# Optimization experiments

Measured on AMD Instinct MI355X. Metric: run time of the kernel, lower is better.

## Reference

```python
import jax, jax.numpy as jnp
import numpy as np

SCALE, Z, X, Y = 4, 9, 9, 9
INV_SQRT_2PI = 1.0 / np.sqrt(2.0 * np.pi)


def setup_inputs() -> dict:
    key = jax.random.key(0)
    k1, = jax.random.split(key, 1)
    inp = jax.random.normal(k1, (1, 1, 128, 512, 512), dtype=jnp.float32)
    return {
        "inp": inp,
        "mu_z": jnp.asarray(0.0, dtype=jnp.float32),
        "sig_z": jnp.asarray(0.1, dtype=jnp.float32),
        "bet_xy": jnp.asarray(2.0, dtype=jnp.float32),
        "bet_z": jnp.asarray(1.5, dtype=jnp.float32),
    }


def _gen_alf(bet_xy, bet_z):
    # squared distances along each axis; torch's loop overwrites the wrap-around
    # write, so the net result for odd sizes is simply (arange - size//2)**2
    zd = ((jnp.arange(Z) - Z // 2) ** 2).astype(jnp.float32)[:, None, None]
    xd = ((jnp.arange(X) - X // 2) ** 2).astype(jnp.float32)[None, :, None]
    yd = ((jnp.arange(Y) - Y // 2) ** 2).astype(jnp.float32)[None, None, :]
    d_2 = zd / bet_z ** 2 + (xd + yd) / bet_xy ** 2  # (Z, X, Y)
    return jnp.exp(-d_2 / 2) * INV_SQRT_2PI


def reference(inp, mu_z, sig_z, bet_xy, bet_z):
    z0 = jnp.exp(mu_z + 0.5 * sig_z ** 2)
    rec = inp * z0  # (N, 1, D, H, W)
    alf = _gen_alf(bet_xy, bet_z)[None, None]  # (1, 1, Z, X, Y)
    pad_z = (Z - SCALE + 1) // 2
    rec = jax.lax.conv_general_dilated(
        rec, alf,
        window_strides=(SCALE, 1, 1),
        padding=[(pad_z, pad_z), (X // 2, X // 2), (Y // 2, Y // 2)],
        dimension_numbers=("NCDHW", "OIDHW", "NCDHW"),
    )  # (N, 1, D//SCALE, H, W)
    rec = (rec - rec.min()) / (rec.max() - rec.min())
    return rec
```

## Files before the change

kernel.cpp:

```cpp
#include <hip/hip_runtime.h>

#define D_IN  128
#define D_OUT 32
#define H     512
#define W     512
#define W4    128
#define HB    8
#define ZR    (HB + 8)
#define NTHR  512
#define CONV_GRID (D_OUT * (H / HB))

__global__ __launch_bounds__(NTHR)
void conv3d_fused(const float* __restrict__ inp, float* __restrict__ out,
                  const float* __restrict__ bxy_p, const float* __restrict__ bz_p,
                  float* __restrict__ blkMin, float* __restrict__ blkMax) {
    __shared__ float zbuf[ZR * W];
    __shared__ float smin[8], smax[8];

    const int d  = blockIdx.x >> 6;
    const int h0 = (blockIdx.x & 63) * HB;

    const float bz = bz_p[0], bx = bxy_p[0];
    const float iz = 1.0f / (2.0f * bz * bz);
    const float ix = 1.0f / (2.0f * bx * bx);
    float wz[9], wx[9];
#pragma unroll
    for (int k = 0; k < 9; ++k) {
        float dd = (float)(k - 4);
        wz[k] = expf(-dd * dd * iz);
        wx[k] = expf(-dd * dd * ix);
    }

    const float4* in4 = (const float4*)inp;
    float4* z4 = (float4*)zbuf;

    for (int t = threadIdx.x; t < ZR * W4; t += NTHR) {
        int r  = t >> 7;
        int c4 = t & (W4 - 1);
        int h  = h0 - 4 + r;
        float4 acc = make_float4(0.f, 0.f, 0.f, 0.f);
        if ((unsigned)h < H) {
            int base = h * W4 + c4;
#pragma unroll
            for (int k = 0; k < 9; ++k) {
                int din = 4 * d - 3 + k;
                if ((unsigned)din < D_IN) {
                    float4 v = in4[din * (H * W4) + base];
                    acc.x += v.x * wz[k]; acc.y += v.y * wz[k];
                    acc.z += v.z * wz[k]; acc.w += v.w * wz[k];
                }
            }
        }
        z4[t] = acc;
    }
    __syncthreads();

    const int lane = threadIdx.x & 63;
    float lmin =  3.402823466e38f;
    float lmax = -3.402823466e38f;
    float4* out4 = (float4*)out;

    for (int t = threadIdx.x; t < HB * W4; t += NTHR) {
        int r  = t >> 7;
        int c4 = t & (W4 - 1);

        float4 v = make_float4(0.f, 0.f, 0.f, 0.f);
#pragma unroll
        for (int k = 0; k < 9; ++k) {
            float4 z = z4[(r + k) * W4 + c4];
            v.x += z.x * wx[k]; v.y += z.y * wx[k];
            v.z += z.z * wx[k]; v.w += z.w * wx[k];
        }

        float4 va, vc;
        va.x = __shfl_up(v.x, 1, 64);  va.y = __shfl_up(v.y, 1, 64);
        va.z = __shfl_up(v.z, 1, 64);  va.w = __shfl_up(v.w, 1, 64);
        vc.x = __shfl_down(v.x, 1, 64); vc.y = __shfl_down(v.y, 1, 64);
        vc.z = __shfl_down(v.z, 1, 64); vc.w = __shfl_down(v.w, 1, 64);

        if (lane == 0 || lane == 63) {
            int c4n = c4 + ((lane == 0) ? -1 : 1);
            float4 vn = make_float4(0.f, 0.f, 0.f, 0.f);
            if ((unsigned)c4n < W4) {
#pragma unroll
                for (int k = 0; k < 9; ++k) {
                    float4 z = z4[(r + k) * W4 + c4n];
                    vn.x += z.x * wx[k]; vn.y += z.y * wx[k];
                    vn.z += z.z * wx[k]; vn.w += z.w * wx[k];
                }
            }
            if (lane == 0) va = vn; else vc = vn;
        }

        float win[12] = {va.x, va.y, va.z, va.w,
                         v.x,  v.y,  v.z,  v.w,
                         vc.x, vc.y, vc.z, vc.w};
        float4 o = make_float4(0.f, 0.f, 0.f, 0.f);
#pragma unroll
        for (int k = 0; k < 9; ++k) {
            o.x += win[k]     * wx[k];
            o.y += win[k + 1] * wx[k];
            o.z += win[k + 2] * wx[k];
            o.w += win[k + 3] * wx[k];
        }
        out4[(d * H + h0 + r) * W4 + c4] = o;
        lmin = fminf(lmin, fminf(fminf(o.x, o.y), fminf(o.z, o.w)));
        lmax = fmaxf(lmax, fmaxf(fmaxf(o.x, o.y), fmaxf(o.z, o.w)));
    }

#pragma unroll
    for (int off = 32; off > 0; off >>= 1) {
        lmin = fminf(lmin, __shfl_down(lmin, off, 64));
        lmax = fmaxf(lmax, __shfl_down(lmax, off, 64));
    }
    int wv = threadIdx.x >> 6;
    if (lane == 0) { smin[wv] = lmin; smax[wv] = lmax; }
    __syncthreads();
    if (threadIdx.x == 0) {
        float mn = smin[0], mx = smax[0];
#pragma unroll
        for (int i = 1; i < 8; ++i) { mn = fminf(mn, smin[i]); mx = fmaxf(mx, smax[i]); }
        blkMin[blockIdx.x] = mn;
        blkMax[blockIdx.x] = mx;
    }
}

#define NORM_NTHR  256
#define NORM_F4_PER_THR 4
#define NORM_GRID  ((D_OUT * H * W4) / (NORM_NTHR * NORM_F4_PER_THR))

__global__ __launch_bounds__(NORM_NTHR)
void norm_kernel(const float* __restrict__ in, float* __restrict__ out,
                 const float* __restrict__ blkMin, const float* __restrict__ blkMax) {
    float lmin =  3.402823466e38f;
    float lmax = -3.402823466e38f;
    for (int i = threadIdx.x; i < CONV_GRID; i += NORM_NTHR) {
        lmin = fminf(lmin, blkMin[i]);
        lmax = fmaxf(lmax, blkMax[i]);
    }
#pragma unroll
    for (int off = 32; off > 0; off >>= 1) {
        lmin = fminf(lmin, __shfl_down(lmin, off, 64));
        lmax = fmaxf(lmax, __shfl_down(lmax, off, 64));
    }
    __shared__ float smin[4], smax[4];
    int lane = threadIdx.x & 63, wv = threadIdx.x >> 6;
    if (lane == 0) { smin[wv] = lmin; smax[wv] = lmax; }
    __syncthreads();
    float mn  = fminf(fminf(smin[0], smin[1]), fminf(smin[2], smin[3]));
    float mx  = fmaxf(fmaxf(smax[0], smax[1]), fmaxf(smax[2], smax[3]));
    float inv = 1.0f / (mx - mn);

    const float4* in4  = (const float4*)in;
    float4*       out4 = (float4*)out;
    int base = blockIdx.x * (NORM_NTHR * NORM_F4_PER_THR) + threadIdx.x;
#pragma unroll
    for (int j = 0; j < NORM_F4_PER_THR; ++j) {
        int idx = base + j * NORM_NTHR;
        float4 v = in4[idx];
        out4[idx] = make_float4((v.x - mn) * inv, (v.y - mn) * inv,
                                (v.z - mn) * inv, (v.w - mn) * inv);
    }
}

extern "C" void kernel_launch(void* const* d_in, const int* in_sizes, int n_in,
                              void* d_out, int out_size, void* d_ws, size_t ws_size,
                              hipStream_t stream) {
    const float* inp    = (const float*)d_in[0];
    const float* bet_xy = (const float*)d_in[3];
    const float* bet_z  = (const float*)d_in[4];
    float* out = (float*)d_out;

    char* ws = (char*)d_ws;
    float* blkMin = (float*)(ws + 4096);
    float* blkMax = (float*)(ws + 16384);
    float* bufA   = (float*)(ws + 65536);

    conv3d_fused<<<CONV_GRID, NTHR, 0, stream>>>(inp, bufA, bet_xy, bet_z, blkMin, blkMax);
    norm_kernel<<<NORM_GRID, NORM_NTHR, 0, stream>>>(bufA, out, blkMin, blkMax);
}
```

Baseline: 255.9 us.

## Stream z-slices through registers and compute several output depths per block

Result: slower. 262.1 us (+2.4%).

```diff
diff --git a/kernel.cpp b/kernel.cpp
--- a/kernel.cpp
+++ b/kernel.cpp
@@ -5,10 +5,12 @@
 #define H     512
 #define W     512
 #define W4    128
-#define HB    8
+#define HB    16
 #define ZR    (HB + 8)
 #define NTHR  512
-#define CONV_GRID (D_OUT * (H / HB))
+#define CD    4
+#define ZCH   (D_OUT / CD)
+#define CONV_GRID (ZCH * (H / HB))
 
 __global__ __launch_bounds__(NTHR)
 void conv3d_fused(const float* __restrict__ inp, float* __restrict__ out,
@@ -17,8 +19,9 @@
     __shared__ float zbuf[ZR * W];
     __shared__ float smin[8], smax[8];
 
-    const int d  = blockIdx.x >> 6;
-    const int h0 = (blockIdx.x & 63) * HB;
+    const int tid = threadIdx.x;
+    const int h0 = (blockIdx.x & 31) * HB;
+    const int d0 = (blockIdx.x >> 5) * CD;
 
     const float bz = bz_p[0], bx = bxy_p[0];
     const float iz = 1.0f / (2.0f * bz * bz);
@@ -34,78 +37,139 @@
     const float4* in4 = (const float4*)inp;
     float4* z4 = (float4*)zbuf;
 
-    for (int t = threadIdx.x; t < ZR * W4; t += NTHR) {
-        int r  = t >> 7;
-        int c4 = t & (W4 - 1);
-        int h  = h0 - 4 + r;
-        float4 acc = make_float4(0.f, 0.f, 0.f, 0.f);
-        if ((unsigned)h < H) {
-            int base = h * W4 + c4;
-#pragma unroll
-            for (int k = 0; k < 9; ++k) {
-                int din = 4 * d - 3 + k;
-                if ((unsigned)din < D_IN) {
-                    float4 v = in4[din * (H * W4) + base];
-                    acc.x += v.x * wz[k]; acc.y += v.y * wz[k];
-                    acc.z += v.z * wz[k]; acc.w += v.w * wz[k];
-                }
-            }
+    int  rowOff[6];
+    bool rowOk[6];
+#pragma unroll
+    for (int j = 0; j < 6; ++j) {
+        int pos = j * NTHR + tid;
+        int r   = pos >> 7;
+        int c4  = pos & (W4 - 1);
+        int h   = h0 - 4 + r;
+        rowOk[j]  = (unsigned)h < H;
+        rowOff[j] = h * W4 + c4;
+    }
+
+    const float4 f4z = make_float4(0.f, 0.f, 0.f, 0.f);
+
+    auto loadSlice = [&](int din, float4 (&v)[6]) {
+        if ((unsigned)din < D_IN) {
+            const float4* p = in4 + (size_t)din * (H * W4);
+#pragma unroll
+            for (int j = 0; j < 6; ++j)
+                v[j] = rowOk[j] ? p[rowOff[j]] : f4z;
+        } else {
+#pragma unroll
+            for (int j = 0; j < 6; ++j) v[j] = f4z;
         }
-        z4[t] = acc;
-    }
-    __syncthreads();
+    };
+    auto fmaSet = [&](float4 (&A)[6], const float4 (&v)[6], float w) {
+#pragma unroll
+        for (int j = 0; j < 6; ++j) {
+            A[j].x += v[j].x * w; A[j].y += v[j].y * w;
+            A[j].z += v[j].z * w; A[j].w += v[j].w * w;
+        }
+    };
+
+    float4 A0[6], A1[6], A2[6];
+#pragma unroll
+    for (int j = 0; j < 6; ++j) A0[j] = A1[j] = A2[j] = f4z;
+
+    const int z0 = 4 * d0 - 3;
+    float4 va[6], vb[6];
+
+    loadSlice(z0 + 0, va);
+    loadSlice(z0 + 1, vb);
+    fmaSet(A0, va, wz[0]);
+    loadSlice(z0 + 2, va);
+    fmaSet(A0, vb, wz[1]);
+    loadSlice(z0 + 3, vb);
+    fmaSet(A0, va, wz[2]);
+    loadSlice(z0 + 4, va);
+    fmaSet(A0, vb, wz[3]);
+    fmaSet(A0, va, wz[4]);
+    fmaSet(A1, va, wz[0]);
 
     const int lane = threadIdx.x & 63;
     float lmin =  3.402823466e38f;
     float lmax = -3.402823466e38f;
     float4* out4 = (float4*)out;
 
-    for (int t = threadIdx.x; t < HB * W4; t += NTHR) {
-        int r  = t >> 7;
-        int c4 = t & (W4 - 1);
-
-        float4 v = make_float4(0.f, 0.f, 0.f, 0.f);
-#pragma unroll
-        for (int k = 0; k < 9; ++k) {
-            float4 z = z4[(r + k) * W4 + c4];
-            v.x += z.x * wx[k]; v.y += z.y * wx[k];
-            v.z += z.z * wx[k]; v.w += z.w * wx[k];
+#pragma unroll
+    for (int i = 0; i < CD; ++i) {
+        const int d = d0 + i;
+        float4 (&Ac)[6]  = (i % 3 == 0) ? A0 : (i % 3 == 1) ? A1 : A2;
+        float4 (&An)[6]  = ((i + 1) % 3 == 0) ? A0 : ((i + 1) % 3 == 1) ? A1 : A2;
+        float4 (&An2)[6] = ((i + 2) % 3 == 0) ? A0 : ((i + 2) % 3 == 1) ? A1 : A2;
+
+        const int b = 4 * d + 2;
+        loadSlice(b + 0, va);
+        loadSlice(b + 1, vb);
+        fmaSet(Ac, va, wz[5]);
+        if (i + 1 < CD) fmaSet(An, va, wz[1]);
+        loadSlice(b + 2, va);
+        fmaSet(Ac, vb, wz[6]);
+        if (i + 1 < CD) fmaSet(An, vb, wz[2]);
+        loadSlice(b + 3, vb);
+        fmaSet(Ac, va, wz[7]);
+        if (i + 1 < CD) fmaSet(An, va, wz[3]);
+        fmaSet(Ac, vb, wz[8]);
+        if (i + 1 < CD) fmaSet(An, vb, wz[4]);
+        if (i + 2 < CD) fmaSet(An2, vb, wz[0]);
+
+        __syncthreads();
+#pragma unroll
+        for (int j = 0; j < 6; ++j) z4[j * NTHR + tid] = Ac[j];
+#pragma unroll
+        for (int j = 0; j < 6; ++j) Ac[j] = f4z;
+        __syncthreads();
+
+        for (int t = tid; t < HB * W4; t += NTHR) {
+            int r  = t >> 7;
+            int c4 = t & (W4 - 1);
+
+            float4 v = f4z;
+#pragma unroll
+            for (int k = 0; k < 9; ++k) {
+                float4 z = z4[(r + k) * W4 + c4];
+                v.x += z.x * wx[k]; v.y += z.y * wx[k];
+                v.z += z.z * wx[k]; v.w += z.w * wx[k];
+            }
+
+            float4 vaw, vcw;
+            vaw.x = __shfl_up(v.x, 1, 64);   vaw.y = __shfl_up(v.y, 1, 64);
+            vaw.z = __shfl_up(v.z, 1, 64);   vaw.w = __shfl_up(v.w, 1, 64);
+            vcw.x = __shfl_down(v.x, 1, 64); vcw.y = __shfl_down(v.y, 1, 64);
+            vcw.z = __shfl_down(v.z, 1, 64); vcw.w = __shfl_down(v.w, 1, 64);
+
+            if (lane == 0 || lane == 63) {
+                int c4n = c4 + ((lane == 0) ? -1 : 1);
+                float4 vn = f4z;
+                if ((unsigned)c4n < W4) {
+#pragma unroll
+                    for (int k = 0; k < 9; ++k) {
+                        float4 z = z4[(r + k) * W4 + c4n];
+                        vn.x += z.x * wx[k]; vn.y += z.y * wx[k];
+                        vn.z += z.z * wx[k]; vn.w += z.w * wx[k];
+                    }
+                }
+                if (lane == 0) vaw = vn; else vcw = vn;
+            }
+
+            float win[12] = {vaw.x, vaw.y, vaw.z, vaw.w,
+                             v.x,   v.y,   v.z,   v.w,
+                             vcw.x, vcw.y, vcw.z, vcw.w};
+            float4 o = f4z;
+#pragma unroll
+            for (int k = 0; k < 9; ++k) {
+                o.x += win[k]     * wx[k];
+                o.y += win[k + 1] * wx[k];
+                o.z += win[k + 2] * wx[k];
+                o.w += win[k + 3] * wx[k];
+            }
+            out4[(d * H + h0 + r) * W4 + c4] = o;
+            lmin = fminf(lmin, fminf(fminf(o.x, o.y), fminf(o.z, o.w)));
+            lmax = fmaxf(lmax, fmaxf(fmaxf(o.x, o.y), fmaxf(o.z, o.w)));
         }
-
-        float4 va, vc;
-        va.x = __shfl_up(v.x, 1, 64);  va.y = __shfl_up(v.y, 1, 64);
-        va.z = __shfl_up(v.z, 1, 64);  va.w = __shfl_up(v.w, 1, 64);
-        vc.x = __shfl_down(v.x, 1, 64); vc.y = __shfl_down(v.y, 1, 64);
-        vc.z = __shfl_down(v.z, 1, 64); vc.w = __shfl_down(v.w, 1, 64);
-
-        if (lane == 0 || lane == 63) {
-            int c4n = c4 + ((lane == 0) ? -1 : 1);
-            float4 vn = make_float4(0.f, 0.f, 0.f, 0.f);
-            if ((unsigned)c4n < W4) {
-#pragma unroll
-                for (int k = 0; k < 9; ++k) {
-                    float4 z = z4[(r + k) * W4 + c4n];
-                    vn.x += z.x * wx[k]; vn.y += z.y * wx[k];
-                    vn.z += z.z * wx[k]; vn.w += z.w * wx[k];
-                }
-            }
-            if (lane == 0) va = vn; else vc = vn;
-        }
-
-        float win[12] = {va.x, va.y, va.z, va.w,
-                         v.x,  v.y,  v.z,  v.w,
-                         vc.x, vc.y, vc.z, vc.w};
-        float4 o = make_float4(0.f, 0.f, 0.f, 0.f);
-#pragma unroll
-        for (int k = 0; k < 9; ++k) {
-            o.x += win[k]     * wx[k];
-            o.y += win[k + 1] * wx[k];
-            o.z += win[k + 2] * wx[k];
-            o.w += win[k + 3] * wx[k];
-        }
-        out4[(d * H + h0 + r) * W4 + c4] = o;
-        lmin = fminf(lmin, fminf(fminf(o.x, o.y), fminf(o.z, o.w)));
-        lmax = fmaxf(lmax, fmaxf(fmaxf(o.x, o.y), fmaxf(o.z, o.w)));
     }
 
 #pragma unroll
```
